# Optimization experiments

Measured on AMD Instinct MI355X. Metric: run time of the kernel, lower is better.

Reference implementation:

```python
import jax, jax.numpy as jnp
import numpy as np

M_GROUPS = 512  # fixed number of segments (== fill_max for ii)


def setup_inputs() -> dict:
    key = jax.random.key(0)
    ks = jax.random.split(key, 8)
    B, N, D = 4, 16384, 384
    x = jax.random.normal(ks[0], (B, N, D), dtype=jnp.float32)
    ii = jax.random.randint(ks[1], (N,), 0, M_GROUPS)
    s = 1.0 / np.sqrt(D)
    f_w = jax.random.uniform(ks[2], (D, D), jnp.float32, -s, s)
    f_b = jax.random.uniform(ks[3], (D,), jnp.float32, -s, s)
    g_w = jax.random.uniform(ks[4], (D, D), jnp.float32, -s, s)
    g_b = jax.random.uniform(ks[5], (D,), jnp.float32, -s, s)
    h_w = jax.random.uniform(ks[6], (D, D), jnp.float32, -s, s)
    h_b = jax.random.uniform(ks[7], (D,), jnp.float32, -s, s)
    return {"x": x, "ii": ii, "f_w": f_w, "f_b": f_b,
            "g_w": g_w, "g_b": g_b, "h_w": h_w, "h_b": h_b}


def reference(x, ii, f_w, f_b, g_w, g_b, h_w, h_b):
    # x: [B, N, D], ii: [N] group indices in [0, M_GROUPS)
    logits = x @ g_w.T + g_b                      # g(x): [B, N, D]
    exp_logits = jnp.exp(logits)
    # segment sum over n for each group m (== one-hot einsum 'bnm,bnd->bmd')
    seg = lambda e: jax.ops.segment_sum(e, ii, num_segments=M_GROUPS)
    sum_exp = jax.vmap(seg)(exp_logits)           # [B, M, D]
    denom = sum_exp[:, ii]                        # gather back: [B, N, D]
    w = exp_logits / (denom + 1e-6)
    fx = x @ f_w.T + f_b                          # f(x): [B, N, D]
    y = jax.vmap(seg)(fx * w)                     # [B, M, D]
    y = y @ h_w.T + h_b                           # h(y)
    return y[:, ii]                               # expand: [B, N, D]
```

## Files before the change

kernel.cpp:

```cpp
#include <hip/hip_runtime.h>
#include <hip/hip_bf16.h>

#define D 384
#define NROWS 16384
#define BATCH 4
#define MG 512
#define RTOT (BATCH * NROWS)
#define NC (2 * D)
#define JB 64
#define NJB (D / JB)
#define BM 128
#define BK 32
#define NKT (D / BK)
#define NMT (RTOT / BM)

typedef __attribute__((ext_vector_type(8))) short bf16x8;
typedef __attribute__((ext_vector_type(4))) float f32x4;

static __device__ __forceinline__ unsigned short f2bf(float f) {
  unsigned int u = __float_as_uint(f);
  unsigned int r = u + 0x7fffu + ((u >> 16) & 1u);
  return (unsigned short)(r >> 16);
}
static __device__ __forceinline__ float bf2f(unsigned short h) {
  return __uint_as_float(((unsigned int)h) << 16);
}

typedef __attribute__((address_space(1))) const void gvoid_t;
typedef __attribute__((address_space(3))) void lvoid_t;
static __device__ __forceinline__ void gl16(const void* g, void* l) {
  __builtin_amdgcn_global_load_lds((gvoid_t*)g, (lvoid_t*)l, 16, 0, 0);
}

__global__ void k_convert_x(const float* __restrict__ x, unsigned short* __restrict__ xb) {
  const long total4 = (long)RTOT * D / 4;
  for (long i = blockIdx.x * (long)blockDim.x + threadIdx.x; i < total4;
       i += (long)gridDim.x * blockDim.x) {
    float4 v = ((const float4*)x)[i];
    ushort4 o;
    o.x = f2bf(v.x); o.y = f2bf(v.y); o.z = f2bf(v.z); o.w = f2bf(v.w);
    ((ushort4*)xb)[i] = o;
  }
}

__global__ void k_build_w(const float* __restrict__ g_w, const float* __restrict__ f_w,
                          const float* __restrict__ h_w,
                          unsigned short* __restrict__ wt2, unsigned short* __restrict__ hw) {
  const int totW = NC * D, totH = D * D;
  int tid0 = blockIdx.x * blockDim.x + threadIdx.x;
  int stride = gridDim.x * blockDim.x;
  for (int idx = tid0; idx < totW; idx += stride) {
    int jblk = idx / (128 * D);
    int rem = idx % (128 * D);
    int c = rem / D, k = rem % D;
    int j = jblk * JB + (c & 63);
    float v = (c < JB) ? g_w[j * D + k] : f_w[j * D + k];
    wt2[idx] = f2bf(v);
  }
  for (int idx = tid0; idx < totH; idx += stride) hw[idx] = f2bf(h_w[idx]);
}

__global__ void k_csr(const int* __restrict__ ii, int* __restrict__ csr_start,
                      int* __restrict__ csr_rows, int* __restrict__ grp_sorted) {
  __shared__ int cnt[MG];
  int t = threadIdx.x;
  cnt[t] = 0;
  __syncthreads();
  for (int n = t; n < NROWS; n += MG) atomicAdd(&cnt[ii[n]], 1);
  __syncthreads();
  if (t == 0) {
    int run = 0;
    for (int i = 0; i < MG; i++) {
      int c = cnt[i];
      cnt[i] = run;
      csr_start[i] = run;
      run += c;
    }
    csr_start[MG] = run;
  }
  __syncthreads();
  for (int n = t; n < NROWS; n += MG) {
    int m = ii[n];
    int pos = atomicAdd(&cnt[m], 1);
    csr_rows[pos] = n;
    grp_sorted[pos] = m;
  }
}

__global__ __launch_bounds__(256, 4) void k_gemm1(
    const unsigned short* __restrict__ xb, const unsigned short* __restrict__ wt2,
    const float* __restrict__ g_b, const float* __restrict__ f_b,
    const int* __restrict__ csr_rows, const int* __restrict__ grp_sorted,
    float* __restrict__ s1acc, float* __restrict__ s2acc) {
  __shared__ __attribute__((aligned(16))) unsigned short As[2][BM * BK];
  __shared__ __attribute__((aligned(16))) unsigned short Bs[2][BM * BK];
  __shared__ int grpS[BM];

  const int wg = blockIdx.x;
  const int xcd = wg & 7;
  const int ix = wg >> 3;
  const int mt = xcd * (NMT / 8) + ix / NJB;
  const int jb = ix % NJB;
  const int b = mt >> 7;
  const int ib = (mt & 127) * BM;
  const int j0 = jb * JB;

  const int tid = threadIdx.x;
  const int lane = tid & 63, wid = tid >> 6;
  const int wr = wid >> 1, wc = wid & 1;

  if (tid < BM) grpS[tid] = grp_sorted[ib + tid];

  const int srow = wid * 32 + (lane >> 2);
  const int skb = (lane & 3) * 16;
  const int arow0 = b * NROWS + csr_rows[ib + srow];
  const int arow1 = b * NROWS + csr_rows[ib + srow + 16];
  const char* aS0 = (const char*)xb + (size_t)arow0 * (D * 2) + skb;
  const char* aS1 = (const char*)xb + (size_t)arow1 * (D * 2) + skb;
  const char* bS0 = (const char*)wt2 + (size_t)jb * (128 * D * 2) + (size_t)srow * (D * 2) + skb;
  const char* bS1 = bS0 + 16 * (D * 2);

  f32x4 acc[4][4];
#pragma unroll
  for (int m = 0; m < 4; m++)
#pragma unroll
    for (int n = 0; n < 4; n++) acc[m][n] = (f32x4){0.f, 0.f, 0.f, 0.f};

  {
    char* ad = (char*)As[0] + wid * 2048;
    char* bd = (char*)Bs[0] + wid * 2048;
    gl16(aS0, ad); gl16(aS1, ad + 1024);
    gl16(bS0, bd); gl16(bS1, bd + 1024);
  }
  __syncthreads();

#pragma unroll 1
  for (int kt = 0; kt < NKT; ++kt) {
    const int cur = kt & 1;
    if (kt < NKT - 1) {
      const int kb = (kt + 1) * (BK * 2);
      char* ad = (char*)As[cur ^ 1] + wid * 2048;
      char* bd = (char*)Bs[cur ^ 1] + wid * 2048;
      gl16(aS0 + kb, ad); gl16(aS1 + kb, ad + 1024);
      gl16(bS0 + kb, bd); gl16(bS1 + kb, bd + 1024);
    }
    bf16x8 af[4], bfv[4];
#pragma unroll
    for (int m = 0; m < 4; m++)
      af[m] = *(const bf16x8*)(&As[cur][(wr * 64 + m * 16 + (lane & 15)) * BK + (lane >> 4) * 8]);
#pragma unroll
    for (int n = 0; n < 4; n++) {
      const int c = (n < 2) ? (wc * 32 + n * 16) : (64 + wc * 32 + (n - 2) * 16);
      bfv[n] = *(const bf16x8*)(&Bs[cur][(c + (lane & 15)) * BK + (lane >> 4) * 8]);
    }
#pragma unroll
    for (int m = 0; m < 4; m++)
#pragma unroll
      for (int n = 0; n < 4; n++)
        acc[m][n] = __builtin_amdgcn_mfma_f32_16x16x32_bf16(af[m], bfv[n], acc[m][n], 0, 0, 0);
    __syncthreads();
  }

  const int jc = lane & 15;
  const int jA = j0 + wc * 32 + jc;
  const float gb0 = g_b[jA], gb1 = g_b[jA + 16];
  const float fb0 = f_b[jA], fb1 = f_b[jA + 16];

  int gmr[4][4];
#pragma unroll
  for (int m = 0; m < 4; m++)
#pragma unroll
    for (int r = 0; r < 4; r++)
      gmr[m][r] = grpS[wr * 64 + m * 16 + (lane >> 4) * 4 + r];

#pragma unroll
  for (int m = 0; m < 4; m++)
#pragma unroll
    for (int r = 0; r < 4; r++) {
      const float e0 = expf(acc[m][0][r] + gb0);
      const float e1 = expf(acc[m][1][r] + gb1);
      const float f0 = acc[m][2][r] + fb0;
      const float f1 = acc[m][3][r] + fb1;
      acc[m][0][r] = e0; acc[m][1][r] = e1;
      acc[m][2][r] = f0 * e0; acc[m][3][r] = f1 * e1;
    }

  const int gLo = grpS[wr * 64], gHi = grpS[wr * 64 + 63];
  for (int g = gLo; g <= gHi; ++g) {
    float v0 = 0.f, v1 = 0.f, v2 = 0.f, v3 = 0.f;
#pragma unroll
    for (int m = 0; m < 4; m++)
#pragma unroll
      for (int r = 0; r < 4; r++)
        if (gmr[m][r] == g) {
          v0 += acc[m][0][r]; v1 += acc[m][1][r];
          v2 += acc[m][2][r]; v3 += acc[m][3][r];
        }
    v0 += __shfl_xor(v0, 16); v0 += __shfl_xor(v0, 32);
    v1 += __shfl_xor(v1, 16); v1 += __shfl_xor(v1, 32);
    v2 += __shfl_xor(v2, 16); v2 += __shfl_xor(v2, 32);
    v3 += __shfl_xor(v3, 16); v3 += __shfl_xor(v3, 32);
    if (lane < 16) {
      float* s1p = s1acc + ((size_t)(b * MG + g)) * D + j0 + wc * 32 + lane;
      float* s2p = s2acc + ((size_t)(b * MG + g)) * D + j0 + wc * 32 + lane;
      atomicAdd(s1p, v0);
      atomicAdd(s1p + 16, v1);
      atomicAdd(s2p, v2);
      atomicAdd(s2p + 16, v3);
    }
  }
}

__global__ __launch_bounds__(256) void k_norm(const float* __restrict__ s1,
                                              const float* __restrict__ s2,
                                              unsigned short* __restrict__ ypre) {
  const int i = blockIdx.x * blockDim.x + threadIdx.x;
  ypre[i] = f2bf(s2[i] / (s1[i] + 1e-6f));
}

__global__ __launch_bounds__(256) void k_gemm2(
    const unsigned short* __restrict__ ypre, const unsigned short* __restrict__ hw,
    const float* __restrict__ h_b, float* __restrict__ outpre) {
  const int tid = threadIdx.x, lane = tid & 63, wid = tid >> 6;
  const int r0 = blockIdx.y * 16;
  const int c0 = blockIdx.x * 64 + wid * 16;
  f32x4 acc = (f32x4){0.f, 0.f, 0.f, 0.f};
  const unsigned short* aRow = ypre + (size_t)(r0 + (lane & 15)) * D + (lane >> 4) * 8;
  const unsigned short* bRow = hw + (size_t)(c0 + (lane & 15)) * D + (lane >> 4) * 8;
#pragma unroll
  for (int kt = 0; kt < D / 32; kt++) {
    bf16x8 af = *(const bf16x8*)(aRow + kt * 32);
    bf16x8 bf_ = *(const bf16x8*)(bRow + kt * 32);
    acc = __builtin_amdgcn_mfma_f32_16x16x32_bf16(af, bf_, acc, 0, 0, 0);
  }
  const int col = c0 + (lane & 15);
  const float hb = h_b[col];
#pragma unroll
  for (int r = 0; r < 4; r++) {
    const int row = r0 + (lane >> 4) * 4 + r;
    outpre[(size_t)row * D + col] = acc[r] + hb;
  }
}

__global__ void k_gather(const float* __restrict__ outpre, const int* __restrict__ ii,
                         float* __restrict__ out) {
  const long total4 = (long)RTOT * (D / 4);
  for (long i = blockIdx.x * (long)blockDim.x + threadIdx.x; i < total4;
       i += (long)gridDim.x * blockDim.x) {
    const long row = i / (D / 4);
    const int q = (int)(i % (D / 4));
    const int b = (int)(row >> 14);
    const int n = (int)(row & (NROWS - 1));
    const int g = ii[n];
    ((float4*)out)[i] = ((const float4*)outpre)[((size_t)(b * MG + g)) * (D / 4) + q];
  }
}

extern "C" void kernel_launch(void* const* d_in, const int* in_sizes, int n_in,
                              void* d_out, int out_size, void* d_ws, size_t ws_size,
                              hipStream_t stream) {
  const float* x = (const float*)d_in[0];
  const int* ii = (const int*)d_in[1];
  const float* f_w = (const float*)d_in[2];
  const float* f_b = (const float*)d_in[3];
  const float* g_w = (const float*)d_in[4];
  const float* g_b = (const float*)d_in[5];
  const float* h_w = (const float*)d_in[6];
  const float* h_b = (const float*)d_in[7];
  float* out = (float*)d_out;

  char* ws = (char*)d_ws;
  size_t off = 0;
  auto alloc = [&](size_t bytes) {
    size_t p = off;
    off = (off + bytes + 255) & ~(size_t)255;
    return p;
  };
  unsigned short* xb = (unsigned short*)(ws + alloc((size_t)RTOT * D * 2));
  unsigned short* wt2 = (unsigned short*)(ws + alloc((size_t)NC * D * 2));
  unsigned short* hw = (unsigned short*)(ws + alloc((size_t)D * D * 2));
  float* s1acc = (float*)(ws + alloc((size_t)BATCH * MG * D * 4));
  float* s2acc = (float*)(ws + alloc((size_t)BATCH * MG * D * 4));
  unsigned short* ypre = (unsigned short*)(ws + alloc((size_t)BATCH * MG * D * 2));
  float* outpre = (float*)(ws + alloc((size_t)BATCH * MG * D * 4));
  int* csr_start = (int*)(ws + alloc((MG + 1) * 4));
  int* csr_rows = (int*)(ws + alloc((size_t)NROWS * 4));
  int* grp_sorted = (int*)(ws + alloc((size_t)NROWS * 4));

  hipMemsetAsync(s1acc, 0, (size_t)2 * BATCH * MG * D * 4, stream);

  k_convert_x<<<dim3(4096), dim3(256), 0, stream>>>(x, xb);
  k_build_w<<<dim3(1152), dim3(256), 0, stream>>>(g_w, f_w, h_w, wt2, hw);
  k_csr<<<dim3(1), dim3(MG), 0, stream>>>(ii, csr_start, csr_rows, grp_sorted);
  k_gemm1<<<dim3(NJB * NMT), dim3(256), 0, stream>>>(xb, wt2, g_b, f_b, csr_rows,
                                                     grp_sorted, s1acc, s2acc);
  k_norm<<<dim3((BATCH * MG * D) / 256), dim3(256), 0, stream>>>(s1acc, s2acc, ypre);
  k_gemm2<<<dim3(D / 64, (BATCH * MG) / 16), dim3(256), 0, stream>>>(ypre, hw, h_b, outpre);
  k_gather<<<dim3(4096), dim3(256), 0, stream>>>(outpre, ii, out);
}
```

Measured before the change: 160.8 us.

## Fuse x bf16 conversion into GEMM1 loads and normalization into GEMM2

```diff
diff --git a/kernel.cpp b/kernel.cpp
--- a/kernel.cpp
+++ b/kernel.cpp
@@ -22,25 +22,21 @@
   unsigned int r = u + 0x7fffu + ((u >> 16) & 1u);
   return (unsigned short)(r >> 16);
 }
-static __device__ __forceinline__ float bf2f(unsigned short h) {
-  return __uint_as_float(((unsigned int)h) << 16);
+static __device__ __forceinline__ unsigned int cvtpk(float lo, float hi) {
+  unsigned int r;
+  asm("v_cvt_pk_bf16_f32 %0, %1, %2" : "=v"(r) : "v"(lo), "v"(hi));
+  return r;
+}
+static __device__ __forceinline__ float frcp(float f) {
+  float r;
+  asm("v_rcp_f32 %0, %1" : "=v"(r) : "v"(f));
+  return r;
 }
 
 typedef __attribute__((address_space(1))) const void gvoid_t;
 typedef __attribute__((address_space(3))) void lvoid_t;
 static __device__ __forceinline__ void gl16(const void* g, void* l) {
   __builtin_amdgcn_global_load_lds((gvoid_t*)g, (lvoid_t*)l, 16, 0, 0);
-}
-
-__global__ void k_convert_x(const float* __restrict__ x, unsigned short* __restrict__ xb) {
-  const long total4 = (long)RTOT * D / 4;
-  for (long i = blockIdx.x * (long)blockDim.x + threadIdx.x; i < total4;
-       i += (long)gridDim.x * blockDim.x) {
-    float4 v = ((const float4*)x)[i];
-    ushort4 o;
-    o.x = f2bf(v.x); o.y = f2bf(v.y); o.z = f2bf(v.z); o.w = f2bf(v.w);
-    ((ushort4*)xb)[i] = o;
-  }
 }
 
 __global__ void k_build_w(const float* __restrict__ g_w, const float* __restrict__ f_w,
@@ -63,21 +59,26 @@
 __global__ void k_csr(const int* __restrict__ ii, int* __restrict__ csr_start,
                       int* __restrict__ csr_rows, int* __restrict__ grp_sorted) {
   __shared__ int cnt[MG];
-  int t = threadIdx.x;
+  __shared__ int scan[MG];
+  const int t = threadIdx.x;
   cnt[t] = 0;
   __syncthreads();
   for (int n = t; n < NROWS; n += MG) atomicAdd(&cnt[ii[n]], 1);
   __syncthreads();
-  if (t == 0) {
-    int run = 0;
-    for (int i = 0; i < MG; i++) {
-      int c = cnt[i];
-      cnt[i] = run;
-      csr_start[i] = run;
-      run += c;
-    }
-    csr_start[MG] = run;
-  }
+  const int v = cnt[t];
+  scan[t] = v;
+  __syncthreads();
+#pragma unroll
+  for (int o = 1; o < MG; o <<= 1) {
+    int u = (t >= o) ? scan[t - o] : 0;
+    __syncthreads();
+    scan[t] += u;
+    __syncthreads();
+  }
+  const int excl = scan[t] - v;
+  csr_start[t] = excl;
+  if (t == MG - 1) csr_start[MG] = scan[t];
+  cnt[t] = excl;
   __syncthreads();
   for (int n = t; n < NROWS; n += MG) {
     int m = ii[n];
@@ -88,7 +89,7 @@
 }
 
 __global__ __launch_bounds__(256, 4) void k_gemm1(
-    const unsigned short* __restrict__ xb, const unsigned short* __restrict__ wt2,
+    const float* __restrict__ x, const unsigned short* __restrict__ wt2,
     const float* __restrict__ g_b, const float* __restrict__ f_b,
     const int* __restrict__ csr_rows, const int* __restrict__ grp_sorted,
     float* __restrict__ s1acc, float* __restrict__ s2acc) {
@@ -112,12 +113,12 @@
   if (tid < BM) grpS[tid] = grp_sorted[ib + tid];
 
   const int srow = wid * 32 + (lane >> 2);
-  const int skb = (lane & 3) * 16;
   const int arow0 = b * NROWS + csr_rows[ib + srow];
   const int arow1 = b * NROWS + csr_rows[ib + srow + 16];
-  const char* aS0 = (const char*)xb + (size_t)arow0 * (D * 2) + skb;
-  const char* aS1 = (const char*)xb + (size_t)arow1 * (D * 2) + skb;
-  const char* bS0 = (const char*)wt2 + (size_t)jb * (128 * D * 2) + (size_t)srow * (D * 2) + skb;
+  const char* aS0 = (const char*)x + (size_t)arow0 * (D * 4) + (lane & 3) * 32;
+  const char* aS1 = (const char*)x + (size_t)arow1 * (D * 4) + (lane & 3) * 32;
+  const char* bS0 = (const char*)wt2 + (size_t)jb * (128 * D * 2) + (size_t)srow * (D * 2) +
+                    (lane & 3) * 16;
   const char* bS1 = bS0 + 16 * (D * 2);
 
   f32x4 acc[4][4];
@@ -126,23 +127,38 @@
 #pragma unroll
     for (int n = 0; n < 4; n++) acc[m][n] = (f32x4){0.f, 0.f, 0.f, 0.f};
 
+  float4 a00 = *(const float4*)(aS0);
+  float4 a01 = *(const float4*)(aS0 + 16);
+  float4 a10 = *(const float4*)(aS1);
+  float4 a11 = *(const float4*)(aS1 + 16);
   {
-    char* ad = (char*)As[0] + wid * 2048;
     char* bd = (char*)Bs[0] + wid * 2048;
-    gl16(aS0, ad); gl16(aS1, ad + 1024);
-    gl16(bS0, bd); gl16(bS1, bd + 1024);
+    gl16(bS0, bd);
+    gl16(bS1, bd + 1024);
+    int4 p0, p1;
+    p0.x = cvtpk(a00.x, a00.y); p0.y = cvtpk(a00.z, a00.w);
+    p0.z = cvtpk(a01.x, a01.y); p0.w = cvtpk(a01.z, a01.w);
+    p1.x = cvtpk(a10.x, a10.y); p1.y = cvtpk(a10.z, a10.w);
+    p1.z = cvtpk(a11.x, a11.y); p1.w = cvtpk(a11.z, a11.w);
+    *(int4*)((char*)As[0] + wid * 2048 + lane * 16) = p0;
+    *(int4*)((char*)As[0] + wid * 2048 + 1024 + lane * 16) = p1;
   }
   __syncthreads();
 
 #pragma unroll 1
   for (int kt = 0; kt < NKT; ++kt) {
     const int cur = kt & 1;
-    if (kt < NKT - 1) {
-      const int kb = (kt + 1) * (BK * 2);
-      char* ad = (char*)As[cur ^ 1] + wid * 2048;
+    const bool more = (kt < NKT - 1);
+    if (more) {
+      const int kbf = (kt + 1) * (BK * 4);
+      const int kbb = (kt + 1) * (BK * 2);
+      a00 = *(const float4*)(aS0 + kbf);
+      a01 = *(const float4*)(aS0 + kbf + 16);
+      a10 = *(const float4*)(aS1 + kbf);
+      a11 = *(const float4*)(aS1 + kbf + 16);
       char* bd = (char*)Bs[cur ^ 1] + wid * 2048;
-      gl16(aS0 + kb, ad); gl16(aS1 + kb, ad + 1024);
-      gl16(bS0 + kb, bd); gl16(bS1 + kb, bd + 1024);
+      gl16(bS0 + kbb, bd);
+      gl16(bS1 + kbb, bd + 1024);
     }
     bf16x8 af[4], bfv[4];
 #pragma unroll
@@ -158,6 +174,15 @@
 #pragma unroll
       for (int n = 0; n < 4; n++)
         acc[m][n] = __builtin_amdgcn_mfma_f32_16x16x32_bf16(af[m], bfv[n], acc[m][n], 0, 0, 0);
+    if (more) {
+      int4 p0, p1;
+      p0.x = cvtpk(a00.x, a00.y); p0.y = cvtpk(a00.z, a00.w);
+      p0.z = cvtpk(a01.x, a01.y); p0.w = cvtpk(a01.z, a01.w);
+      p1.x = cvtpk(a10.x, a10.y); p1.y = cvtpk(a10.z, a10.w);
+      p1.z = cvtpk(a11.x, a11.y); p1.w = cvtpk(a11.z, a11.w);
+      *(int4*)((char*)As[cur ^ 1] + wid * 2048 + lane * 16) = p0;
+      *(int4*)((char*)As[cur ^ 1] + wid * 2048 + 1024 + lane * 16) = p1;
+    }
     __syncthreads();
   }
 
@@ -211,25 +236,30 @@
   }
 }
 
-__global__ __launch_bounds__(256) void k_norm(const float* __restrict__ s1,
-                                              const float* __restrict__ s2,
-                                              unsigned short* __restrict__ ypre) {
-  const int i = blockIdx.x * blockDim.x + threadIdx.x;
-  ypre[i] = f2bf(s2[i] / (s1[i] + 1e-6f));
-}
-
 __global__ __launch_bounds__(256) void k_gemm2(
-    const unsigned short* __restrict__ ypre, const unsigned short* __restrict__ hw,
-    const float* __restrict__ h_b, float* __restrict__ outpre) {
+    const float* __restrict__ s1, const float* __restrict__ s2,
+    const unsigned short* __restrict__ hw, const float* __restrict__ h_b,
+    float* __restrict__ outpre) {
   const int tid = threadIdx.x, lane = tid & 63, wid = tid >> 6;
   const int r0 = blockIdx.y * 16;
   const int c0 = blockIdx.x * 64 + wid * 16;
   f32x4 acc = (f32x4){0.f, 0.f, 0.f, 0.f};
-  const unsigned short* aRow = ypre + (size_t)(r0 + (lane & 15)) * D + (lane >> 4) * 8;
+  const int arow = r0 + (lane & 15);
+  const float* s1p = s1 + (size_t)arow * D + (lane >> 4) * 8;
+  const float* s2p = s2 + (size_t)arow * D + (lane >> 4) * 8;
   const unsigned short* bRow = hw + (size_t)(c0 + (lane & 15)) * D + (lane >> 4) * 8;
 #pragma unroll
   for (int kt = 0; kt < D / 32; kt++) {
-    bf16x8 af = *(const bf16x8*)(aRow + kt * 32);
+    float4 u0 = *(const float4*)(s1p + kt * 32);
+    float4 u1 = *(const float4*)(s1p + kt * 32 + 4);
+    float4 w0 = *(const float4*)(s2p + kt * 32);
+    float4 w1 = *(const float4*)(s2p + kt * 32 + 4);
+    int4 yi;
+    yi.x = cvtpk(w0.x * frcp(u0.x + 1e-6f), w0.y * frcp(u0.y + 1e-6f));
+    yi.y = cvtpk(w0.z * frcp(u0.z + 1e-6f), w0.w * frcp(u0.w + 1e-6f));
+    yi.z = cvtpk(w1.x * frcp(u1.x + 1e-6f), w1.y * frcp(u1.y + 1e-6f));
+    yi.w = cvtpk(w1.z * frcp(u1.z + 1e-6f), w1.w * frcp(u1.w + 1e-6f));
+    bf16x8 af = *(bf16x8*)&yi;
     bf16x8 bf_ = *(const bf16x8*)(bRow + kt * 32);
     acc = __builtin_amdgcn_mfma_f32_16x16x32_bf16(af, bf_, acc, 0, 0, 0);
   }
@@ -276,12 +306,10 @@
     off = (off + bytes + 255) & ~(size_t)255;
     return p;
   };
-  unsigned short* xb = (unsigned short*)(ws + alloc((size_t)RTOT * D * 2));
   unsigned short* wt2 = (unsigned short*)(ws + alloc((size_t)NC * D * 2));
   unsigned short* hw = (unsigned short*)(ws + alloc((size_t)D * D * 2));
   float* s1acc = (float*)(ws + alloc((size_t)BATCH * MG * D * 4));
   float* s2acc = (float*)(ws + alloc((size_t)BATCH * MG * D * 4));
-  unsigned short* ypre = (unsigned short*)(ws + alloc((size_t)BATCH * MG * D * 2));
   float* outpre = (float*)(ws + alloc((size_t)BATCH * MG * D * 4));
   int* csr_start = (int*)(ws + alloc((MG + 1) * 4));
   int* csr_rows = (int*)(ws + alloc((size_t)NROWS * 4));
@@ -289,12 +317,11 @@
 
   hipMemsetAsync(s1acc, 0, (size_t)2 * BATCH * MG * D * 4, stream);
 
-  k_convert_x<<<dim3(4096), dim3(256), 0, stream>>>(x, xb);
   k_build_w<<<dim3(1152), dim3(256), 0, stream>>>(g_w, f_w, h_w, wt2, hw);
   k_csr<<<dim3(1), dim3(MG), 0, stream>>>(ii, csr_start, csr_rows, grp_sorted);
-  k_gemm1<<<dim3(NJB * NMT), dim3(256), 0, stream>>>(xb, wt2, g_b, f_b, csr_rows,
+  k_gemm1<<<dim3(NJB * NMT), dim3(256), 0, stream>>>(x, wt2, g_b, f_b, csr_rows,
                                                      grp_sorted, s1acc, s2acc);
-  k_norm<<<dim3((BATCH * MG * D) / 256), dim3(256), 0, stream>>>(s1acc, s2acc, ypre);
-  k_gemm2<<<dim3(D / 64, (BATCH * MG) / 16), dim3(256), 0, stream>>>(ypre, hw, h_b, outpre);
+  k_gemm2<<<dim3(D / 64, (BATCH * MG) / 16), dim3(256), 0, stream>>>(s1acc, s2acc, hw, h_b,
+                                                                     outpre);
   k_gather<<<dim3(4096), dim3(256), 0, stream>>>(outpre, ii, out);
 }
```

After: 146.6 us. 1.1x faster.
